# Optimization experiments

Hardware: AMD Instinct MI355X
Metric: run time of the kernel (lower is better)

## Reference

```python
import jax, jax.numpy as jnp
import numpy as np

N_STEPS = 3            # n_internal_steps
USE_CURRENT_ACTIVS = True
LEAKY_SLOPE = 0.01     # F.leaky_relu default


def _apply_act(x, ids):
    # per-node activation lookup: 0=identity 1=leaky_relu 2=relu 3=sigmoid 4=tanh
    return jnp.select(
        [ids == 0, ids == 1, ids == 2, ids == 3],
        [x,
         jnp.where(x >= 0, x, LEAKY_SLOPE * x),
         jnp.maximum(x, jnp.zeros((), x.dtype)),
         jax.nn.sigmoid(x)],
        jnp.tanh(x))


def setup_inputs() -> dict:
    key = jax.random.key(0)
    ks = jax.random.split(key, 14)
    B, NI, NH, NO = 1, 4096, 8192, 2048
    s = 0.02  # keep recurrent dynamics stable
    return {
        "inputs": jax.random.normal(ks[0], (B, NI), jnp.float32),
        "W_i2h": jax.random.normal(ks[1], (NH, NI), jnp.float32) * s,
        "W_h2h": jax.random.normal(ks[2], (NH, NH), jnp.float32) * s,
        "W_o2h": jax.random.normal(ks[3], (NH, NO), jnp.float32) * s,
        "W_i2o": jax.random.normal(ks[4], (NO, NI), jnp.float32) * s,
        "W_h2o": jax.random.normal(ks[5], (NO, NH), jnp.float32) * s,
        "W_o2o": jax.random.normal(ks[6], (NO, NO), jnp.float32) * s,
        "hidden_responses": jax.random.uniform(ks[7], (NH,), jnp.float32, 0.5, 1.5),
        "hidden_biases": jax.random.normal(ks[8], (NH,), jnp.float32) * 0.1,
        "output_responses": jax.random.uniform(ks[9], (NO,), jnp.float32, 0.5, 1.5),
        "output_biases": jax.random.normal(ks[10], (NO,), jnp.float32) * 0.1,
        "activs0": jnp.zeros((B, NH), jnp.float32),
        "outputs0": jnp.zeros((B, NO), jnp.float32),
        "hidden_act_ids": jax.random.randint(ks[11], (NH,), 0, 5, jnp.int32),
        "output_act_ids": jax.random.randint(ks[12], (NO,), 0, 5, jnp.int32),
    }


def reference(inputs, W_i2h, W_h2h, W_o2h, W_i2o, W_h2o, W_o2o,
              hidden_responses, hidden_biases, output_responses, output_biases,
              activs0, outputs0, hidden_act_ids, output_act_ids):
    activs = activs0          # (B, NH) recurrent hidden state
    outputs = outputs0        # (B, NO) recurrent output state
    activs_for_output = activs
    for _ in range(N_STEPS):
        pre = hidden_responses * (inputs @ W_i2h.T
                                  + activs @ W_h2h.T
                                  + outputs @ W_o2h.T) + hidden_biases
        activs = _apply_act(pre, hidden_act_ids[None, :])
    if USE_CURRENT_ACTIVS:
        activs_for_output = activs
    out_in = inputs @ W_i2o.T + outputs @ W_o2o.T + activs_for_output @ W_h2o.T
    pre_out = output_responses * out_in + output_biases
    return _apply_act(pre_out, output_act_ids[None, :])
```

## Files before the change

### kernel.cpp

```cpp
#include <hip/hip_runtime.h>

#define NI 4096
#define NH 8192
#define NO 2048

typedef float f4 __attribute__((ext_vector_type(4)));

__device__ __forceinline__ float apply_act(float x, int id) {
    switch (id) {
        case 0:  return x;
        case 1:  return x >= 0.f ? x : 0.01f * x;
        case 2:  return fmaxf(x, 0.f);
        case 3:  return 1.f / (1.f + expf(-x));
        default: return tanhf(x);
    }
}

template <bool NT>
__device__ __forceinline__ float wave_dot(const float* __restrict__ Wrow,
                                          const float* __restrict__ x,
                                          int K, int lane) {
    const f4* __restrict__ W4 = (const f4*)Wrow;
    const f4* __restrict__ x4 = (const f4*)x;
    float acc = 0.f;
    const int n4 = K >> 2;
    #pragma unroll 4
    for (int i = lane; i < n4; i += 64) {
        f4 w = NT ? __builtin_nontemporal_load(W4 + i) : W4[i];
        f4 v = x4[i];
        acc = fmaf(w.x, v.x, acc);
        acc = fmaf(w.y, v.y, acc);
        acc = fmaf(w.z, v.z, acc);
        acc = fmaf(w.w, v.w, acc);
    }
    #pragma unroll
    for (int off = 32; off; off >>= 1) acc += __shfl_xor(acc, off, 64);
    return acc;
}

__global__ __launch_bounds__(256) void k_flags(const float* __restrict__ xin,
                                               const float* __restrict__ a0,
                                               const float* __restrict__ o0,
                                               int* __restrict__ flags) {
    __shared__ int s[3];
    int t = threadIdx.x;
    if (t < 3) s[t] = 0;
    __syncthreads();
    int f0 = 0, f1 = 0, f2 = 0;
    for (int i = t; i < NI; i += 256) f0 |= (xin[i] != 0.f);
    for (int i = t; i < NH; i += 256) f1 |= (a0[i]  != 0.f);
    for (int i = t; i < NO; i += 256) f2 |= (o0[i]  != 0.f);
    if (f0) atomicOr(&s[0], 1);
    if (f1) atomicOr(&s[1], 1);
    if (f2) atomicOr(&s[2], 1);
    __syncthreads();
    if (t < 3) flags[t] = s[t];
}

__global__ __launch_bounds__(256) void k_h_init(const float* __restrict__ W_i2h,
                                                const float* __restrict__ W_o2h,
                                                const float* __restrict__ W_h2h,
                                                const float* __restrict__ xin,
                                                const float* __restrict__ o0,
                                                const float* __restrict__ a0,
                                                const float* __restrict__ resp,
                                                const float* __restrict__ bias,
                                                const int* __restrict__ ids,
                                                const int* __restrict__ flags,
                                                float* __restrict__ c_h,
                                                float* __restrict__ act_a) {
    int wave = threadIdx.x >> 6;
    int lane = threadIdx.x & 63;
    int m = blockIdx.x * 4 + wave;
    float c = 0.f;
    if (flags[0]) c += wave_dot<true>(W_i2h + (size_t)m * NI, xin, NI, lane);
    if (flags[2]) c += wave_dot<true>(W_o2h + (size_t)m * NO, o0,  NO, lane);
    float d = 0.f;
    if (flags[1]) d = wave_dot<false>(W_h2h + (size_t)m * NH, a0, NH, lane);
    if (lane == 0) {
        c_h[m] = c;
        act_a[m] = apply_act(fmaf(resp[m], c + d, bias[m]), ids[m]);
    }
}

template <int REV>
__global__ __launch_bounds__(256) void k_step(const float* __restrict__ W_h2h,
                                              const float* __restrict__ x,
                                              const float* __restrict__ c_h,
                                              const float* __restrict__ resp,
                                              const float* __restrict__ bias,
                                              const int* __restrict__ ids,
                                              float* __restrict__ out) {
    int wave = threadIdx.x >> 6;
    int lane = threadIdx.x & 63;
    int m = blockIdx.x * 4 + wave;
    if (REV) m = (NH - 1) - m;
    float dot = wave_dot<false>(W_h2h + (size_t)m * NH, x, NH, lane);
    if (lane == 0) {
        float pre = fmaf(resp[m], c_h[m] + dot, bias[m]);
        out[m] = apply_act(pre, ids[m]);
    }
}

__global__ __launch_bounds__(256) void k_final(const float* __restrict__ W_i2o,
                                               const float* __restrict__ W_o2o,
                                               const float* __restrict__ W_h2o,
                                               const float* __restrict__ xin,
                                               const float* __restrict__ o0,
                                               const float* __restrict__ act,
                                               const float* __restrict__ resp,
                                               const float* __restrict__ bias,
                                               const int* __restrict__ ids,
                                               const int* __restrict__ flags,
                                               float* __restrict__ out) {
    int wave = threadIdx.x >> 6;
    int lane = threadIdx.x & 63;
    int m = blockIdx.x * 4 + wave;
    float dot = wave_dot<true>(W_h2o + (size_t)m * NH, act, NH, lane);
    if (flags[0]) dot += wave_dot<true>(W_i2o + (size_t)m * NI, xin, NI, lane);
    if (flags[2]) dot += wave_dot<true>(W_o2o + (size_t)m * NO, o0,  NO, lane);
    if (lane == 0) {
        float pre = fmaf(resp[m], dot, bias[m]);
        out[m] = apply_act(pre, ids[m]);
    }
}

extern "C" void kernel_launch(void* const* d_in, const int* in_sizes, int n_in,
                              void* d_out, int out_size, void* d_ws, size_t ws_size,
                              hipStream_t stream) {
    const float* inputs   = (const float*)d_in[0];
    const float* W_i2h    = (const float*)d_in[1];
    const float* W_h2h    = (const float*)d_in[2];
    const float* W_o2h    = (const float*)d_in[3];
    const float* W_i2o    = (const float*)d_in[4];
    const float* W_h2o    = (const float*)d_in[5];
    const float* W_o2o    = (const float*)d_in[6];
    const float* h_resp   = (const float*)d_in[7];
    const float* h_bias   = (const float*)d_in[8];
    const float* o_resp   = (const float*)d_in[9];
    const float* o_bias   = (const float*)d_in[10];
    const float* activs0  = (const float*)d_in[11];
    const float* outputs0 = (const float*)d_in[12];
    const int*   h_ids    = (const int*)d_in[13];
    const int*   o_ids    = (const int*)d_in[14];

    float* ws    = (float*)d_ws;
    float* c_h   = ws;
    float* act_a = ws + NH;
    float* act_b = ws + 2 * NH;
    int*   flags = (int*)(ws + 3 * NH);

    k_flags<<<1, 256, 0, stream>>>(inputs, activs0, outputs0, flags);

    k_h_init<<<NH / 4, 256, 0, stream>>>(W_i2h, W_o2h, W_h2h, inputs, outputs0,
                                         activs0, h_resp, h_bias, h_ids, flags,
                                         c_h, act_a);
    k_step<0><<<NH / 4, 256, 0, stream>>>(W_h2h, act_a, c_h, h_resp, h_bias, h_ids,
                                          act_b);
    k_step<1><<<NH / 4, 256, 0, stream>>>(W_h2h, act_b, c_h, h_resp, h_bias, h_ids,
                                          act_a);

    k_final<<<NO / 4, 256, 0, stream>>>(W_i2o, W_o2o, W_h2o, inputs, outputs0, act_a,
                                        o_resp, o_bias, o_ids, flags, (float*)d_out);
}
```

Measured before the change: 134.4 us.

## Convert W_h2h to bf16 during step two and reuse it in step three

```diff
diff --git a/kernel.cpp b/kernel.cpp
--- a/kernel.cpp
+++ b/kernel.cpp
@@ -4,7 +4,9 @@
 #define NH 8192
 #define NO 2048
 
-typedef float f4 __attribute__((ext_vector_type(4)));
+typedef float  f4 __attribute__((ext_vector_type(4)));
+typedef unsigned short u16x8 __attribute__((ext_vector_type(8)));
+typedef unsigned int   u32x2 __attribute__((ext_vector_type(2)));
 
 __device__ __forceinline__ float apply_act(float x, int id) {
     switch (id) {
@@ -14,6 +16,14 @@
         case 3:  return 1.f / (1.f + expf(-x));
         default: return tanhf(x);
     }
+}
+
+__device__ __forceinline__ unsigned int f2bf(float f) {
+    unsigned int u = __float_as_uint(f);
+    return (u + 0x7FFFu + ((u >> 16) & 1u)) >> 16;
+}
+__device__ __forceinline__ float bf2f(unsigned int b) {
+    return __uint_as_float(b << 16);
 }
 
 template <bool NT>
@@ -32,6 +42,32 @@
         acc = fmaf(w.y, v.y, acc);
         acc = fmaf(w.z, v.z, acc);
         acc = fmaf(w.w, v.w, acc);
+    }
+    #pragma unroll
+    for (int off = 32; off; off >>= 1) acc += __shfl_xor(acc, off, 64);
+    return acc;
+}
+
+__device__ __forceinline__ float wave_dot_bf(const unsigned short* __restrict__ Wrow,
+                                             const float* __restrict__ x,
+                                             int K, int lane) {
+    const u16x8* __restrict__ W8 = (const u16x8*)Wrow;
+    const f4* __restrict__ x4 = (const f4*)x;
+    float acc = 0.f;
+    const int n8 = K >> 3;
+    #pragma unroll 4
+    for (int i = lane; i < n8; i += 64) {
+        u16x8 w = W8[i];
+        f4 va = x4[2 * i];
+        f4 vb = x4[2 * i + 1];
+        acc = fmaf(bf2f(w[0]), va.x, acc);
+        acc = fmaf(bf2f(w[1]), va.y, acc);
+        acc = fmaf(bf2f(w[2]), va.z, acc);
+        acc = fmaf(bf2f(w[3]), va.w, acc);
+        acc = fmaf(bf2f(w[4]), vb.x, acc);
+        acc = fmaf(bf2f(w[5]), vb.y, acc);
+        acc = fmaf(bf2f(w[6]), vb.z, acc);
+        acc = fmaf(bf2f(w[7]), vb.w, acc);
     }
     #pragma unroll
     for (int off = 32; off; off >>= 1) acc += __shfl_xor(acc, off, 64);
@@ -80,6 +116,59 @@
     if (lane == 0) {
         c_h[m] = c;
         act_a[m] = apply_act(fmaf(resp[m], c + d, bias[m]), ids[m]);
+    }
+}
+
+__global__ __launch_bounds__(256) void k_step2_conv(const float* __restrict__ W_h2h,
+                                                    const float* __restrict__ x,
+                                                    const float* __restrict__ c_h,
+                                                    const float* __restrict__ resp,
+                                                    const float* __restrict__ bias,
+                                                    const int* __restrict__ ids,
+                                                    float* __restrict__ out,
+                                                    unsigned short* __restrict__ Wb) {
+    int wave = threadIdx.x >> 6;
+    int lane = threadIdx.x & 63;
+    int m = blockIdx.x * 4 + wave;
+    const f4* __restrict__ W4 = (const f4*)(W_h2h + (size_t)m * NH);
+    const f4* __restrict__ x4 = (const f4*)x;
+    u32x2* __restrict__ B2 = (u32x2*)(Wb + (size_t)m * NH);
+    float acc = 0.f;
+    #pragma unroll 4
+    for (int i = lane; i < NH / 4; i += 64) {
+        f4 w = __builtin_nontemporal_load(W4 + i);
+        f4 v = x4[i];
+        acc = fmaf(w.x, v.x, acc);
+        acc = fmaf(w.y, v.y, acc);
+        acc = fmaf(w.z, v.z, acc);
+        acc = fmaf(w.w, v.w, acc);
+        u32x2 b;
+        b.x = f2bf(w.x) | (f2bf(w.y) << 16);
+        b.y = f2bf(w.z) | (f2bf(w.w) << 16);
+        B2[i] = b;
+    }
+    #pragma unroll
+    for (int off = 32; off; off >>= 1) acc += __shfl_xor(acc, off, 64);
+    if (lane == 0) {
+        float pre = fmaf(resp[m], c_h[m] + acc, bias[m]);
+        out[m] = apply_act(pre, ids[m]);
+    }
+}
+
+__global__ __launch_bounds__(256) void k_step3_bf(const unsigned short* __restrict__ Wb,
+                                                  const float* __restrict__ x,
+                                                  const float* __restrict__ c_h,
+                                                  const float* __restrict__ resp,
+                                                  const float* __restrict__ bias,
+                                                  const int* __restrict__ ids,
+                                                  float* __restrict__ out) {
+    int wave = threadIdx.x >> 6;
+    int lane = threadIdx.x & 63;
+    int m = (NH - 1) - (blockIdx.x * 4 + wave);
+    float dot = wave_dot_bf(Wb + (size_t)m * NH, x, NH, lane);
+    if (lane == 0) {
+        float pre = fmaf(resp[m], c_h[m] + dot, bias[m]);
+        out[m] = apply_act(pre, ids[m]);
     }
 }
 
@@ -150,15 +239,26 @@
     float* act_b = ws + 2 * NH;
     int*   flags = (int*)(ws + 3 * NH);
 
+    size_t bf_off = (((size_t)(3 * NH + 4) * sizeof(float)) + 255) & ~(size_t)255;
+    unsigned short* Wb = (unsigned short*)((char*)d_ws + bf_off);
+    bool use_bf = ws_size >= bf_off + (size_t)NH * NH * sizeof(unsigned short);
+
     k_flags<<<1, 256, 0, stream>>>(inputs, activs0, outputs0, flags);
 
     k_h_init<<<NH / 4, 256, 0, stream>>>(W_i2h, W_o2h, W_h2h, inputs, outputs0,
                                          activs0, h_resp, h_bias, h_ids, flags,
                                          c_h, act_a);
-    k_step<0><<<NH / 4, 256, 0, stream>>>(W_h2h, act_a, c_h, h_resp, h_bias, h_ids,
-                                          act_b);
-    k_step<1><<<NH / 4, 256, 0, stream>>>(W_h2h, act_b, c_h, h_resp, h_bias, h_ids,
-                                          act_a);
+    if (use_bf) {
+        k_step2_conv<<<NH / 4, 256, 0, stream>>>(W_h2h, act_a, c_h, h_resp, h_bias,
+                                                 h_ids, act_b, Wb);
+        k_step3_bf<<<NH / 4, 256, 0, stream>>>(Wb, act_b, c_h, h_resp, h_bias,
+                                               h_ids, act_a);
+    } else {
+        k_step<0><<<NH / 4, 256, 0, stream>>>(W_h2h, act_a, c_h, h_resp, h_bias,
+                                              h_ids, act_b);
+        k_step<1><<<NH / 4, 256, 0, stream>>>(W_h2h, act_b, c_h, h_resp, h_bias,
+                                              h_ids, act_a);
+    }
 
     k_final<<<NO / 4, 256, 0, stream>>>(W_i2o, W_o2o, W_h2o, inputs, outputs0, act_a,
                                         o_resp, o_bias, o_ids, flags, (float*)d_out);
```

Result: slower. 143.3 us (+6.6%).

## Compute two rows per wave in step kernels and split-K the final GEMV

Applied to the files above, without the earlier changes.

```diff
diff --git a/kernel.cpp b/kernel.cpp
--- a/kernel.cpp
+++ b/kernel.cpp
@@ -36,6 +36,35 @@
     #pragma unroll
     for (int off = 32; off; off >>= 1) acc += __shfl_xor(acc, off, 64);
     return acc;
+}
+
+template <bool NT>
+__device__ __forceinline__ void wave_dot2(const float* __restrict__ Wr0,
+                                          const float* __restrict__ Wr1,
+                                          const float* __restrict__ x,
+                                          int K, int lane,
+                                          float& d0, float& d1) {
+    const f4* __restrict__ W0 = (const f4*)Wr0;
+    const f4* __restrict__ W1 = (const f4*)Wr1;
+    const f4* __restrict__ x4 = (const f4*)x;
+    float a0 = 0.f, a1 = 0.f;
+    const int n4 = K >> 2;
+    #pragma unroll 4
+    for (int i = lane; i < n4; i += 64) {
+        f4 v = x4[i];
+        f4 w0 = NT ? __builtin_nontemporal_load(W0 + i) : W0[i];
+        f4 w1 = NT ? __builtin_nontemporal_load(W1 + i) : W1[i];
+        a0 = fmaf(w0.x, v.x, a0); a0 = fmaf(w0.y, v.y, a0);
+        a0 = fmaf(w0.z, v.z, a0); a0 = fmaf(w0.w, v.w, a0);
+        a1 = fmaf(w1.x, v.x, a1); a1 = fmaf(w1.y, v.y, a1);
+        a1 = fmaf(w1.z, v.z, a1); a1 = fmaf(w1.w, v.w, a1);
+    }
+    #pragma unroll
+    for (int off = 32; off; off >>= 1) {
+        a0 += __shfl_xor(a0, off, 64);
+        a1 += __shfl_xor(a1, off, 64);
+    }
+    d0 = a0; d1 = a1;
 }
 
 __global__ __launch_bounds__(256) void k_flags(const float* __restrict__ xin,
@@ -83,7 +112,7 @@
     }
 }
 
-template <int REV>
+template <int STEP>
 __global__ __launch_bounds__(256) void k_step(const float* __restrict__ W_h2h,
                                               const float* __restrict__ x,
                                               const float* __restrict__ c_h,
@@ -93,12 +122,21 @@
                                               float* __restrict__ out) {
     int wave = threadIdx.x >> 6;
     int lane = threadIdx.x & 63;
-    int m = blockIdx.x * 4 + wave;
-    if (REV) m = (NH - 1) - m;
-    float dot = wave_dot<false>(W_h2h + (size_t)m * NH, x, NH, lane);
+    int pair = blockIdx.x * 4 + wave;
+    int m0 = 2 * pair;
+    if (STEP == 1) m0 = (NH - 2) - m0;
+    int m1 = m0 + 1;
+    float d0, d1;
+    if (m0 < NH / 2) {
+        wave_dot2<true >(W_h2h + (size_t)m0 * NH, W_h2h + (size_t)m1 * NH,
+                         x, NH, lane, d0, d1);
+    } else {
+        wave_dot2<false>(W_h2h + (size_t)m0 * NH, W_h2h + (size_t)m1 * NH,
+                         x, NH, lane, d0, d1);
+    }
     if (lane == 0) {
-        float pre = fmaf(resp[m], c_h[m] + dot, bias[m]);
-        out[m] = apply_act(pre, ids[m]);
+        out[m0] = apply_act(fmaf(resp[m0], c_h[m0] + d0, bias[m0]), ids[m0]);
+        out[m1] = apply_act(fmaf(resp[m1], c_h[m1] + d1, bias[m1]), ids[m1]);
     }
 }
 
@@ -113,15 +151,23 @@
                                                const int* __restrict__ ids,
                                                const int* __restrict__ flags,
                                                float* __restrict__ out) {
+    __shared__ float part[4];
     int wave = threadIdx.x >> 6;
     int lane = threadIdx.x & 63;
-    int m = blockIdx.x * 4 + wave;
-    float dot = wave_dot<true>(W_h2o + (size_t)m * NH, act, NH, lane);
-    if (flags[0]) dot += wave_dot<true>(W_i2o + (size_t)m * NI, xin, NI, lane);
-    if (flags[2]) dot += wave_dot<true>(W_o2o + (size_t)m * NO, o0,  NO, lane);
-    if (lane == 0) {
-        float pre = fmaf(resp[m], dot, bias[m]);
-        out[m] = apply_act(pre, ids[m]);
+    int rloc = wave >> 1;
+    int kh   = wave & 1;
+    int m = blockIdx.x * 2 + rloc;
+    float acc = wave_dot<true>(W_h2o + (size_t)m * NH + kh * (NH / 2),
+                               act + kh * (NH / 2), NH / 2, lane);
+    if (kh == 0 && flags[0])
+        acc += wave_dot<true>(W_i2o + (size_t)m * NI, xin, NI, lane);
+    if (kh == 1 && flags[2])
+        acc += wave_dot<true>(W_o2o + (size_t)m * NO, o0, NO, lane);
+    if (lane == 0) part[wave] = acc;
+    __syncthreads();
+    if (kh == 0 && lane == 0) {
+        float dot = part[wave] + part[wave + 1];
+        out[m] = apply_act(fmaf(resp[m], dot, bias[m]), ids[m]);
     }
 }
 
@@ -155,11 +201,11 @@
     k_h_init<<<NH / 4, 256, 0, stream>>>(W_i2h, W_o2h, W_h2h, inputs, outputs0,
                                          activs0, h_resp, h_bias, h_ids, flags,
                                          c_h, act_a);
-    k_step<0><<<NH / 4, 256, 0, stream>>>(W_h2h, act_a, c_h, h_resp, h_bias, h_ids,
+    k_step<0><<<NH / 8, 256, 0, stream>>>(W_h2h, act_a, c_h, h_resp, h_bias, h_ids,
                                           act_b);
-    k_step<1><<<NH / 4, 256, 0, stream>>>(W_h2h, act_b, c_h, h_resp, h_bias, h_ids,
+    k_step<1><<<NH / 8, 256, 0, stream>>>(W_h2h, act_b, c_h, h_resp, h_bias, h_ids,
                                           act_a);
 
-    k_final<<<NO / 4, 256, 0, stream>>>(W_i2o, W_o2o, W_h2o, inputs, outputs0, act_a,
+    k_final<<<NO / 2, 256, 0, stream>>>(W_i2o, W_o2o, W_h2o, inputs, outputs0, act_a,
                                         o_resp, o_bias, o_ids, flags, (float*)d_out);
 }
```

Measured after the change: 155.5 us. 1.16x slower.

## Fuse all recurrent steps into one persistent kernel with grid barriers

Applied to the files above, without the earlier changes.

```diff
diff --git a/kernel.cpp b/kernel.cpp
--- a/kernel.cpp
+++ b/kernel.cpp
@@ -3,6 +3,8 @@
 #define NI 4096
 #define NH 8192
 #define NO 2048
+#define NBLK 512
+#define NWAVE (NBLK * 4)
 
 typedef float f4 __attribute__((ext_vector_type(4)));
 
@@ -38,90 +40,104 @@
     return acc;
 }
 
-__global__ __launch_bounds__(256) void k_flags(const float* __restrict__ xin,
-                                               const float* __restrict__ a0,
-                                               const float* __restrict__ o0,
-                                               int* __restrict__ flags) {
-    __shared__ int s[3];
-    int t = threadIdx.x;
-    if (t < 3) s[t] = 0;
+__device__ __forceinline__ void grid_barrier(int* cnt, int* flag) {
     __syncthreads();
-    int f0 = 0, f1 = 0, f2 = 0;
-    for (int i = t; i < NI; i += 256) f0 |= (xin[i] != 0.f);
-    for (int i = t; i < NH; i += 256) f1 |= (a0[i]  != 0.f);
-    for (int i = t; i < NO; i += 256) f2 |= (o0[i]  != 0.f);
-    if (f0) atomicOr(&s[0], 1);
-    if (f1) atomicOr(&s[1], 1);
-    if (f2) atomicOr(&s[2], 1);
+    if (threadIdx.x == 0) {
+        int old = __hip_atomic_fetch_add(cnt, 1, __ATOMIC_ACQ_REL,
+                                         __HIP_MEMORY_SCOPE_AGENT);
+        if (old == (int)gridDim.x - 1) {
+            __hip_atomic_store(flag, 1, __ATOMIC_RELEASE,
+                               __HIP_MEMORY_SCOPE_AGENT);
+        } else {
+            while (!__hip_atomic_load(flag, __ATOMIC_ACQUIRE,
+                                      __HIP_MEMORY_SCOPE_AGENT))
+                __builtin_amdgcn_s_sleep(1);
+        }
+    }
     __syncthreads();
-    if (t < 3) flags[t] = s[t];
 }
 
-__global__ __launch_bounds__(256) void k_h_init(const float* __restrict__ W_i2h,
-                                                const float* __restrict__ W_o2h,
-                                                const float* __restrict__ W_h2h,
-                                                const float* __restrict__ xin,
-                                                const float* __restrict__ o0,
-                                                const float* __restrict__ a0,
-                                                const float* __restrict__ resp,
-                                                const float* __restrict__ bias,
-                                                const int* __restrict__ ids,
-                                                const int* __restrict__ flags,
-                                                float* __restrict__ c_h,
-                                                float* __restrict__ act_a) {
-    int wave = threadIdx.x >> 6;
-    int lane = threadIdx.x & 63;
-    int m = blockIdx.x * 4 + wave;
-    float c = 0.f;
-    if (flags[0]) c += wave_dot<true>(W_i2h + (size_t)m * NI, xin, NI, lane);
-    if (flags[2]) c += wave_dot<true>(W_o2h + (size_t)m * NO, o0,  NO, lane);
-    float d = 0.f;
-    if (flags[1]) d = wave_dot<false>(W_h2h + (size_t)m * NH, a0, NH, lane);
-    if (lane == 0) {
-        c_h[m] = c;
-        act_a[m] = apply_act(fmaf(resp[m], c + d, bias[m]), ids[m]);
+__global__ __launch_bounds__(256, 2) void k_fused(
+        const float* __restrict__ xin,
+        const float* __restrict__ W_i2h,
+        const float* __restrict__ W_h2h,
+        const float* __restrict__ W_o2h,
+        const float* __restrict__ W_i2o,
+        const float* __restrict__ W_h2o,
+        const float* __restrict__ W_o2o,
+        const float* __restrict__ h_resp,
+        const float* __restrict__ h_bias,
+        const float* __restrict__ o_resp,
+        const float* __restrict__ o_bias,
+        const float* __restrict__ a0,
+        const float* __restrict__ o0,
+        const int* __restrict__ h_ids,
+        const int* __restrict__ o_ids,
+        float* __restrict__ c_h,
+        float* __restrict__ act_a,
+        float* __restrict__ act_b,
+        float* __restrict__ act_c,
+        int* __restrict__ flags,
+        int* __restrict__ bar,
+        float* __restrict__ out) {
+    const int wave = threadIdx.x >> 6;
+    const int lane = threadIdx.x & 63;
+    const int gw = blockIdx.x * 4 + wave;
+
+    {
+        int gtid = blockIdx.x * 256 + threadIdx.x;
+        int gsz = NBLK * 256;
+        int f0 = 0, f1 = 0, f2 = 0;
+        for (int i = gtid; i < NI; i += gsz) f0 |= (xin[i] != 0.f);
+        for (int i = gtid; i < NH; i += gsz) f1 |= (a0[i]  != 0.f);
+        for (int i = gtid; i < NO; i += gsz) f2 |= (o0[i]  != 0.f);
+        if (__any(f0) && lane == 0) atomicOr(flags + 0, 1);
+        if (__any(f1) && lane == 0) atomicOr(flags + 1, 1);
+        if (__any(f2) && lane == 0) atomicOr(flags + 2, 1);
     }
-}
+    grid_barrier(bar + 0, bar + 4);
+    const int f0 = flags[0], f1 = flags[1], f2 = flags[2];
 
-template <int REV>
-__global__ __launch_bounds__(256) void k_step(const float* __restrict__ W_h2h,
-                                              const float* __restrict__ x,
-                                              const float* __restrict__ c_h,
-                                              const float* __restrict__ resp,
-                                              const float* __restrict__ bias,
-                                              const int* __restrict__ ids,
-                                              float* __restrict__ out) {
-    int wave = threadIdx.x >> 6;
-    int lane = threadIdx.x & 63;
-    int m = blockIdx.x * 4 + wave;
-    if (REV) m = (NH - 1) - m;
-    float dot = wave_dot<false>(W_h2h + (size_t)m * NH, x, NH, lane);
-    if (lane == 0) {
-        float pre = fmaf(resp[m], c_h[m] + dot, bias[m]);
-        out[m] = apply_act(pre, ids[m]);
+    #pragma unroll
+    for (int p = 0; p < NH / NWAVE; ++p) {
+        int m = gw + p * NWAVE;
+        float c = 0.f;
+        if (f0) c += wave_dot<true>(W_i2h + (size_t)m * NI, xin, NI, lane);
+        if (f2) c += wave_dot<true>(W_o2h + (size_t)m * NO, o0,  NO, lane);
+        float d = 0.f;
+        if (f1) d = wave_dot<true>(W_h2h + (size_t)m * NH, a0, NH, lane);
+        if (lane == 0) {
+            c_h[m] = c;
+            act_a[m] = apply_act(fmaf(h_resp[m], c + d, h_bias[m]), h_ids[m]);
+        }
     }
-}
+    grid_barrier(bar + 1, bar + 5);
 
-__global__ __launch_bounds__(256) void k_final(const float* __restrict__ W_i2o,
-                                               const float* __restrict__ W_o2o,
-                                               const float* __restrict__ W_h2o,
-                                               const float* __restrict__ xin,
-                                               const float* __restrict__ o0,
-                                               const float* __restrict__ act,
-                                               const float* __restrict__ resp,
-                                               const float* __restrict__ bias,
-                                               const int* __restrict__ ids,
-                                               const int* __restrict__ flags,
-                                               float* __restrict__ out) {
-    int wave = threadIdx.x >> 6;
-    int lane = threadIdx.x & 63;
-    int m = blockIdx.x * 4 + wave;
-    float dot = wave_dot<true>(W_h2o + (size_t)m * NH, act, NH, lane);
-    if (flags[0]) dot += wave_dot<true>(W_i2o + (size_t)m * NI, xin, NI, lane);
-    if (flags[2]) dot += wave_dot<true>(W_o2o + (size_t)m * NO, o0,  NO, lane);
-    if (lane == 0) {
-        float pre = fmaf(resp[m], dot, bias[m]);
-        out[m] = apply_act(pre, ids[m]);
+    #pragma unroll
+    for (int p = 0; p < NH / NWAVE; ++p) {
+        int m = gw + p * NWAVE;
+        float d = wave_dot<true>(W_h2h + (size_t)m * NH, act_a, NH, lane);
+        if (lane == 0)
+            act_b[m] = apply_act(fmaf(h_resp[m], c_h[m] + d, h_bias[m]), h_ids[m]);
+    }
+    grid_barrier(bar + 2, bar + 6);
+
+    #pragma unroll
+    for (int p = 0; p < NH / NWAVE; ++p) {
+        int m = gw + p * NWAVE;
+        float d = wave_dot<true>(W_h2h + (size_t)m * NH, act_b, NH, lane);
+        if (lane == 0)
+            act_c[m] = apply_act(fmaf(h_resp[m], c_h[m] + d, h_bias[m]), h_ids[m]);
+    }
+    grid_barrier(bar + 3, bar + 7);
+
+    {
+        int m = gw;
+        float dot = wave_dot<true>(W_h2o + (size_t)m * NH, act_c, NH, lane);
+        if (f0) dot += wave_dot<true>(W_i2o + (size_t)m * NI, xin, NI, lane);
+        if (f2) dot += wave_dot<true>(W_o2o + (size_t)m * NO, o0,  NO, lane);
+        if (lane == 0)
+            out[m] = apply_act(fmaf(o_resp[m], dot, o_bias[m]), o_ids[m]);
     }
 }
 
@@ -148,18 +164,16 @@
     float* c_h   = ws;
     float* act_a = ws + NH;
     float* act_b = ws + 2 * NH;
-    int*   flags = (int*)(ws + 3 * NH);
+    float* act_c = ws + 3 * NH;
+    int*   ints  = (int*)(ws + 4 * NH);
+    int*   flags = ints;
+    int*   bar   = ints + 3;
 
-    k_flags<<<1, 256, 0, stream>>>(inputs, activs0, outputs0, flags);
+    hipMemsetAsync(ints, 0, 11 * sizeof(int), stream);
 
-    k_h_init<<<NH / 4, 256, 0, stream>>>(W_i2h, W_o2h, W_h2h, inputs, outputs0,
-                                         activs0, h_resp, h_bias, h_ids, flags,
-                                         c_h, act_a);
-    k_step<0><<<NH / 4, 256, 0, stream>>>(W_h2h, act_a, c_h, h_resp, h_bias, h_ids,
-                                          act_b);
-    k_step<1><<<NH / 4, 256, 0, stream>>>(W_h2h, act_b, c_h, h_resp, h_bias, h_ids,
-                                          act_a);
-
-    k_final<<<NO / 4, 256, 0, stream>>>(W_i2o, W_o2o, W_h2o, inputs, outputs0, act_a,
-                                        o_resp, o_bias, o_ids, flags, (float*)d_out);
+    k_fused<<<NBLK, 256, 0, stream>>>(inputs, W_i2h, W_h2h, W_o2h, W_i2o, W_h2o,
+                                      W_o2o, h_resp, h_bias, o_resp, o_bias,
+                                      activs0, outputs0, h_ids, o_ids,
+                                      c_h, act_a, act_b, act_c, flags, bar,
+                                      (float*)d_out);
 }
```

Result: slower. 372.2 us (+177.0%).
